# Kernel tuning notes

Measured on AMD Instinct MI355X. Metric: run time of the kernel, lower is better.

## Reference

```python
import jax, jax.numpy as jnp
import numpy as np

N_NODES = 50000
N_EDGES = 800000
D_IN = 128
D_OUT = 128


def setup_inputs() -> dict:
    key = jax.random.key(0)
    ks = jax.random.split(key, 10)
    x = jax.random.normal(ks[0], (N_NODES, D_IN), dtype=jnp.float32)
    lp_rows = jax.random.randint(ks[1], (N_EDGES,), 0, N_NODES, dtype=jnp.int32)
    lp_cols = jax.random.randint(ks[2], (N_EDGES,), 0, N_NODES, dtype=jnp.int32)
    # low-pass operator: positive normalized-adjacency-like weights
    lp_vals = jax.random.uniform(ks[3], (N_EDGES,), dtype=jnp.float32) / 16.0
    hp_rows = jax.random.randint(ks[4], (N_EDGES,), 0, N_NODES, dtype=jnp.int32)
    hp_cols = jax.random.randint(ks[5], (N_EDGES,), 0, N_NODES, dtype=jnp.int32)
    # high-pass operator: signed (Laplacian-like) weights
    hp_vals = jax.random.normal(ks[6], (N_EDGES,), dtype=jnp.float32) / 16.0
    alpha_w = jax.random.normal(ks[7], (1, D_IN), dtype=jnp.float32) * 0.05
    alpha_b = jnp.zeros((1,), dtype=jnp.float32)
    W = jax.random.normal(ks[8], (D_OUT, D_IN), dtype=jnp.float32) * (1.0 / np.sqrt(D_IN))
    b = jnp.zeros((D_OUT,), dtype=jnp.float32)
    return {"x": x, "lp_rows": lp_rows, "lp_cols": lp_cols, "lp_vals": lp_vals,
            "hp_rows": hp_rows, "hp_cols": hp_cols, "hp_vals": hp_vals,
            "alpha_w": alpha_w, "alpha_b": alpha_b, "W": W, "b": b}


def _spmm(rows, cols, vals, x, n):
    # COO sparse-dense matmul: out[r] += vals[e] * x[cols[e]]
    return jax.ops.segment_sum(vals[:, None] * x[cols], rows, num_segments=n)


def reference(x, lp_rows, lp_cols, lp_vals, hp_rows, hp_cols, hp_vals,
              alpha_w, alpha_b, W, b):
    n = x.shape[0]
    # per-node mixing gate: alpha_i = sigmoid(x_i . theta + b)  -> [N, 1]
    alpha = jax.nn.sigmoid(x @ alpha_w.T + alpha_b)
    z_lp = _spmm(lp_rows, lp_cols, lp_vals, x, n)   # [N, D_IN]
    z_hp = _spmm(hp_rows, hp_cols, hp_vals, x, n)   # [N, D_IN]
    z_mix = alpha * z_lp + (1.0 - alpha) * z_hp
    out = jax.nn.relu(z_mix @ W.T + b)              # use_activation=True
    return out, alpha
```

## Files before the change

### kernel.cpp

```cpp
#include <hip/hip_runtime.h>

#define N_NODES_C 50000
#define N_EDGES_C 800000
#define N_EDGES2_C (2 * N_EDGES_C)
#define D 128
#define NSHARD 8
#define SCAP 16
#define OFCAP 4096

#define GNODES 64
#define GP 16
#define LDP 132
#define GRID ((N_NODES_C + GNODES - 1) / GNODES)
#define EPB ((N_EDGES2_C + GRID - 1) / GRID)

static __device__ __forceinline__ unsigned short f2bf(float f) {
  unsigned u = __float_as_uint(f);
  u += 0x7fff + ((u >> 16) & 1);
  return (unsigned short)(u >> 16);
}
static __device__ __forceinline__ float bf_lo(unsigned u) {
  return __uint_as_float(u << 16);
}
static __device__ __forceinline__ float bf_hi(unsigned u) {
  return __uint_as_float(u & 0xffff0000u);
}

static __device__ __forceinline__ int xcd_id() {
  int v;
  asm volatile("s_getreg_b32 %0, hwreg(HW_REG_XCC_ID, 0, 4)" : "=s"(v));
  return v & (NSHARD - 1);
}

__global__ __launch_bounds__(256) void alpha_kernel(
    const float* __restrict__ x,
    const float* __restrict__ aw,
    const float* __restrict__ ab,
    float* __restrict__ alpha_out,
    float* __restrict__ alpha_ws,
    int n) {
  int wave = (int)((blockIdx.x * blockDim.x + threadIdx.x) >> 6);
  int lane = threadIdx.x & 63;
  if (wave >= n) return;
  const float* xr = x + (size_t)wave * D;
  float s = xr[lane] * aw[lane] + xr[lane + 64] * aw[lane + 64];
  #pragma unroll
  for (int off = 32; off > 0; off >>= 1)
    s += __shfl_down(s, off);
  if (lane == 0) {
    float a = 1.0f / (1.0f + __expf(-(s + ab[0])));
    alpha_out[wave] = a;
    alpha_ws[wave] = a;
  }
}

__global__ __launch_bounds__(256) void gemm_fill_kernel(
    const float* __restrict__ x,
    const float* __restrict__ W,
    unsigned* __restrict__ y,
    const int* __restrict__ lp_rows, const int* __restrict__ lp_cols,
    const float* __restrict__ lp_vals,
    const int* __restrict__ hp_rows, const int* __restrict__ hp_cols,
    const float* __restrict__ hp_vals,
    const float* __restrict__ alpha,
    int* __restrict__ rcursor,
    unsigned* __restrict__ pairs,
    int* __restrict__ ofcnt,
    uint2* __restrict__ ofl,
    int n) {
  __shared__ float wt[64][LDP];
  __shared__ float zs[GP][LDP];

  int t = threadIdx.x;
  int node0 = blockIdx.x * GNODES;

  int tj = t >> 3;
  int ns = t & 7;
  int jl = tj * 2;

  for (int jh = 0; jh < 2; ++jh) {
    __syncthreads();
    #pragma unroll
    for (int it = 0; it < 8; ++it) {
      int f = t + it * 256;
      int j = f >> 5;
      int k4 = f & 31;
      *(float4*)&wt[j][k4 * 4] =
          ((const float4*)W)[(size_t)(jh * 64 + j) * 32 + k4];
    }

    for (int p = 0; p < 4; ++p) {
      int nb = node0 + p * GP;
      __syncthreads();
      #pragma unroll
      for (int it = 0; it < 2; ++it) {
        int f = t + it * 256;
        int r = f >> 5;
        int c4 = f & 31;
        int node = nb + r;
        float4 v = make_float4(0.f, 0.f, 0.f, 0.f);
        if (node < n) v = ((const float4*)(x + (size_t)node * D))[c4];
        *(float4*)&zs[r][c4 * 4] = v;
      }
      __syncthreads();

      float acc[2][2] = {};
      #pragma unroll 4
      for (int k = 0; k < D; k += 4) {
        float4 w0 = *(const float4*)&wt[jl][k];
        float4 w1 = *(const float4*)&wt[jl + 1][k];
        float4 z0 = *(const float4*)&zs[ns * 2 + 0][k];
        float4 z1 = *(const float4*)&zs[ns * 2 + 1][k];
        acc[0][0] += z0.x * w0.x + z0.y * w0.y + z0.z * w0.z + z0.w * w0.w;
        acc[0][1] += z0.x * w1.x + z0.y * w1.y + z0.z * w1.z + z0.w * w1.w;
        acc[1][0] += z1.x * w0.x + z1.y * w0.y + z1.z * w0.z + z1.w * w0.w;
        acc[1][1] += z1.x * w1.x + z1.y * w1.y + z1.z * w1.z + z1.w * w1.w;
      }

      #pragma unroll
      for (int ii = 0; ii < 2; ++ii) {
        int node = nb + ns * 2 + ii;
        if (node < n) {
          unsigned o = (unsigned)f2bf(acc[ii][0]) |
                       ((unsigned)f2bf(acc[ii][1]) << 16);
          y[(size_t)node * 64 + jh * 32 + tj] = o;
        }
      }
    }
  }

  int xcc = xcd_id();
  int e0 = blockIdx.x * EPB;
  int e1 = e0 + EPB;
  if (e1 > N_EDGES2_C) e1 = N_EDGES2_C;
  for (int e = e0 + t; e < e1; e += 256) {
    int r, c;
    float v;
    if (e < N_EDGES_C) {
      r = lp_rows[e];
      c = lp_cols[e];
      v = lp_vals[e] * alpha[r];
    } else {
      int i = e - N_EDGES_C;
      r = hp_rows[i];
      c = hp_cols[i];
      v = hp_vals[i] * (1.0f - alpha[r]);
    }
    int p = atomicAdd(&rcursor[xcc * N_NODES_C + r], 1);
    if (p < SCAP) {
      unsigned pk = (unsigned)c | ((unsigned)f2bf(v) << 16);
      pairs[((size_t)r << 7) + (xcc << 4) + p] = pk;
    } else {
      int q = atomicAdd(ofcnt, 1);
      if (q < OFCAP)
        ofl[q] = make_uint2(((unsigned)r << 16) | (unsigned)c,
                            (unsigned)__float_as_int(v));
    }
  }
}

__global__ __launch_bounds__(256) void gather_kernel(
    const int* __restrict__ rcursor,
    const unsigned* __restrict__ pairs,
    const unsigned* __restrict__ y,
    const float* __restrict__ bias,
    const int* __restrict__ ofcnt,
    const uint2* __restrict__ ofl,
    float* __restrict__ out) {
  __shared__ float2 part[4][64];
  int t = threadIdx.x;
  int w = t >> 6;
  int lane = t & 63;
  int row = blockIdx.x * 2 + (w >> 1);
  int half = w & 1;

  float aL = 0.f, aH = 0.f;
  if (row < N_NODES_C) {
    const unsigned* rp = pairs + ((size_t)row << 7) + (half << 6);
    unsigned wsrc = rp[lane];

    #pragma unroll
    for (int sc = 0; sc < 4; ++sc) {
      int s = half * 4 + sc;
      int ds = rcursor[(size_t)s * N_NODES_C + row];
      if (ds > SCAP) ds = SCAP;
      int base = sc << 4;
      int p = 0;
      for (; p + 1 < ds; p += 2) {
        unsigned pk0 = (unsigned)__shfl((int)wsrc, base + p);
        unsigned pk1 = (unsigned)__shfl((int)wsrc, base + p + 1);
        unsigned u0 = y[(size_t)(pk0 & 0xffffu) * 64 + lane];
        unsigned u1 = y[(size_t)(pk1 & 0xffffu) * 64 + lane];
        float v0 = bf_hi(pk0);
        float v1 = bf_hi(pk1);
        aL += v0 * bf_lo(u0) + v1 * bf_lo(u1);
        aH += v0 * bf_hi(u0) + v1 * bf_hi(u1);
      }
      if (p < ds) {
        unsigned pk = (unsigned)__shfl((int)wsrc, base + p);
        unsigned u = y[(size_t)(pk & 0xffffu) * 64 + lane];
        aL += bf_hi(pk) * bf_lo(u);
        aH += bf_hi(pk) * bf_hi(u);
      }
    }

    if (half == 0) {
      int nof = *ofcnt;
      if (nof > OFCAP) nof = OFCAP;
      for (int i = 0; i < nof; ++i) {
        uint2 o = ofl[i];
        if ((int)(o.x >> 16) == row) {
          unsigned u = y[(size_t)(o.x & 0xffffu) * 64 + lane];
          float v = __int_as_float((int)o.y);
          aL += v * bf_lo(u);
          aH += v * bf_hi(u);
        }
      }
    }
  }
  part[w][lane] = make_float2(aL, aH);
  __syncthreads();

  if (half == 0 && row < N_NODES_C) {
    float2 a = part[w][lane];
    float2 b = part[w + 1][lane];
    float2 bv = *(const float2*)&bias[lane * 2];
    float2 o;
    o.x = fmaxf(a.x + b.x + bv.x, 0.0f);
    o.y = fmaxf(a.y + b.y + bv.y, 0.0f);
    *(float2*)&out[(size_t)row * D + lane * 2] = o;
  }
}

extern "C" void kernel_launch(void* const* d_in, const int* in_sizes, int n_in,
                              void* d_out, int out_size, void* d_ws, size_t ws_size,
                              hipStream_t stream) {
  const float* x = (const float*)d_in[0];
  const int* lp_rows = (const int*)d_in[1];
  const int* lp_cols = (const int*)d_in[2];
  const float* lp_vals = (const float*)d_in[3];
  const int* hp_rows = (const int*)d_in[4];
  const int* hp_cols = (const int*)d_in[5];
  const float* hp_vals = (const float*)d_in[6];
  const float* alpha_w = (const float*)d_in[7];
  const float* alpha_b = (const float*)d_in[8];
  const float* W = (const float*)d_in[9];
  const float* bias = (const float*)d_in[10];

  float* out = (float*)d_out;
  float* alpha_out = out + (size_t)N_NODES_C * D;

  char* ws = (char*)d_ws;
  unsigned* y = (unsigned*)ws;   ws += (size_t)N_NODES_C * 64 * 4;
  float* alpha_ws = (float*)ws;  ws += 200192;
  int* rcursor = (int*)ws;       ws += (size_t)N_NODES_C * NSHARD * 4;
  int* ofcnt = (int*)ws;         ws += 256;
  uint2* ofl = (uint2*)ws;       ws += (size_t)OFCAP * 8;
  unsigned* pairs = (unsigned*)ws;
  ws += (size_t)N_NODES_C * NSHARD * SCAP * 4;

  hipMemsetAsync(rcursor, 0,
                 (size_t)N_NODES_C * NSHARD * sizeof(int) + 256, stream);

  alpha_kernel<<<(N_NODES_C + 3) / 4, 256, 0, stream>>>(
      x, alpha_w, alpha_b, alpha_out, alpha_ws, N_NODES_C);

  gemm_fill_kernel<<<GRID, 256, 0, stream>>>(
      x, W, y,
      lp_rows, lp_cols, lp_vals, hp_rows, hp_cols, hp_vals,
      alpha_ws, rcursor, pairs, ofcnt, ofl, N_NODES_C);

  gather_kernel<<<(N_NODES_C + 1) / 2, 256, 0, stream>>>(
      rcursor, pairs, (const unsigned*)y, bias, ofcnt, ofl, out);
}
```

Measured before the change: 319.1 us.

## Split fused GEMM/fill kernel and retile GEMM to 4x4 register blocks

Splits the combined projection-and-edge-bucketing kernel into a dedicated GEMM kernel and a separate fill kernel with its own grid of 2048 blocks. The GEMM now loads all 64 node rows into shared memory once and computes a 4x4 output block per thread, which raises the work per shared-memory load and writes 64-bit packed bf16 results. The aim is better register reuse and occupancy tuned to each phase. The cost is an extra kernel launch, the loss of overlap between GEMM and edge scatter inside one block, and more shared memory per GEMM block.

```diff
diff --git a/kernel.cpp b/kernel.cpp
--- a/kernel.cpp
+++ b/kernel.cpp
@@ -9,10 +9,10 @@
 #define OFCAP 4096
 
 #define GNODES 64
-#define GP 16
 #define LDP 132
-#define GRID ((N_NODES_C + GNODES - 1) / GNODES)
-#define EPB ((N_EDGES2_C + GRID - 1) / GRID)
+#define GGRID ((N_NODES_C + GNODES - 1) / GNODES)
+#define FGRID 2048
+#define FEPB ((N_EDGES2_C + FGRID - 1) / FGRID)
 
 static __device__ __forceinline__ unsigned short f2bf(float f) {
   unsigned u = __float_as_uint(f);
@@ -54,10 +54,86 @@
   }
 }
 
-__global__ __launch_bounds__(256) void gemm_fill_kernel(
+__global__ __launch_bounds__(256) void gemm_kernel(
     const float* __restrict__ x,
     const float* __restrict__ W,
     unsigned* __restrict__ y,
+    int n) {
+  __shared__ float zs[GNODES][LDP];
+  __shared__ float wt[64][LDP];
+
+  int t = threadIdx.x;
+  int node0 = blockIdx.x * GNODES;
+  int tn = t & 15;
+  int tjg = t >> 4;
+  int jb = tjg * 4;
+
+  #pragma unroll
+  for (int it = 0; it < 8; ++it) {
+    int f = t + it * 256;
+    int r = f >> 5;
+    int c4 = f & 31;
+    int node = node0 + r;
+    float4 v = make_float4(0.f, 0.f, 0.f, 0.f);
+    if (node < n) v = ((const float4*)(x + (size_t)node * D))[c4];
+    *(float4*)&zs[r][c4 * 4] = v;
+  }
+
+  for (int jh = 0; jh < 2; ++jh) {
+    if (jh) __syncthreads();
+    #pragma unroll
+    for (int it = 0; it < 8; ++it) {
+      int f = t + it * 256;
+      int j = f >> 5;
+      int k4 = f & 31;
+      *(float4*)&wt[j][k4 * 4] =
+          ((const float4*)W)[(size_t)(jh * 64 + j) * 32 + k4];
+    }
+    __syncthreads();
+
+    float acc[4][4] = {};
+    #pragma unroll 2
+    for (int k = 0; k < D; k += 4) {
+      float4 w0 = *(const float4*)&wt[jb + 0][k];
+      float4 w1 = *(const float4*)&wt[jb + 1][k];
+      float4 w2 = *(const float4*)&wt[jb + 2][k];
+      float4 w3 = *(const float4*)&wt[jb + 3][k];
+      float4 z0 = *(const float4*)&zs[tn][k];
+      float4 z1 = *(const float4*)&zs[tn + 16][k];
+      float4 z2 = *(const float4*)&zs[tn + 32][k];
+      float4 z3 = *(const float4*)&zs[tn + 48][k];
+      acc[0][0] += z0.x*w0.x + z0.y*w0.y + z0.z*w0.z + z0.w*w0.w;
+      acc[0][1] += z0.x*w1.x + z0.y*w1.y + z0.z*w1.z + z0.w*w1.w;
+      acc[0][2] += z0.x*w2.x + z0.y*w2.y + z0.z*w2.z + z0.w*w2.w;
+      acc[0][3] += z0.x*w3.x + z0.y*w3.y + z0.z*w3.z + z0.w*w3.w;
+      acc[1][0] += z1.x*w0.x + z1.y*w0.y + z1.z*w0.z + z1.w*w0.w;
+      acc[1][1] += z1.x*w1.x + z1.y*w1.y + z1.z*w1.z + z1.w*w1.w;
+      acc[1][2] += z1.x*w2.x + z1.y*w2.y + z1.z*w2.z + z1.w*w2.w;
+      acc[1][3] += z1.x*w3.x + z1.y*w3.y + z1.z*w3.z + z1.w*w3.w;
+      acc[2][0] += z2.x*w0.x + z2.y*w0.y + z2.z*w0.z + z2.w*w0.w;
+      acc[2][1] += z2.x*w1.x + z2.y*w1.y + z2.z*w1.z + z2.w*w1.w;
+      acc[2][2] += z2.x*w2.x + z2.y*w2.y + z2.z*w2.z + z2.w*w2.w;
+      acc[2][3] += z2.x*w3.x + z2.y*w3.y + z2.z*w3.z + z2.w*w3.w;
+      acc[3][0] += z3.x*w0.x + z3.y*w0.y + z3.z*w0.z + z3.w*w0.w;
+      acc[3][1] += z3.x*w1.x + z3.y*w1.y + z3.z*w1.z + z3.w*w1.w;
+      acc[3][2] += z3.x*w2.x + z3.y*w2.y + z3.z*w2.z + z3.w*w2.w;
+      acc[3][3] += z3.x*w3.x + z3.y*w3.y + z3.z*w3.z + z3.w*w3.w;
+    }
+
+    #pragma unroll
+    for (int ii = 0; ii < 4; ++ii) {
+      int node = node0 + ii * 16 + tn;
+      if (node < n) {
+        uint2 o;
+        o.x = (unsigned)f2bf(acc[ii][0]) | ((unsigned)f2bf(acc[ii][1]) << 16);
+        o.y = (unsigned)f2bf(acc[ii][2]) | ((unsigned)f2bf(acc[ii][3]) << 16);
+        *(uint2*)&y[(size_t)node * 64 + jh * 32 + tjg * 2] = o;
+      }
+    }
+  }
+}
+
+__global__ __launch_bounds__(256) void fill_kernel(
     const int* __restrict__ lp_rows, const int* __restrict__ lp_cols,
     const float* __restrict__ lp_vals,
     const int* __restrict__ hp_rows, const int* __restrict__ hp_cols,
@@ -66,72 +142,11 @@
     int* __restrict__ rcursor,
     unsigned* __restrict__ pairs,
     int* __restrict__ ofcnt,
-    uint2* __restrict__ ofl,
-    int n) {
-  __shared__ float wt[64][LDP];
-  __shared__ float zs[GP][LDP];
-
+    uint2* __restrict__ ofl) {
+  int xcc = xcd_id();
   int t = threadIdx.x;
-  int node0 = blockIdx.x * GNODES;
-
-  int tj = t >> 3;
-  int ns = t & 7;
-  int jl = tj * 2;
-
-  for (int jh = 0; jh < 2; ++jh) {
-    __syncthreads();
-    #pragma unroll
-    for (int it = 0; it < 8; ++it) {
-      int f = t + it * 256;
-      int j = f >> 5;
-      int k4 = f & 31;
-      *(float4*)&wt[j][k4 * 4] =
-          ((const float4*)W)[(size_t)(jh * 64 + j) * 32 + k4];
-    }
-
-    for (int p = 0; p < 4; ++p) {
-      int nb = node0 + p * GP;
-      __syncthreads();
-      #pragma unroll
-      for (int it = 0; it < 2; ++it) {
-        int f = t + it * 256;
-        int r = f >> 5;
-        int c4 = f & 31;
-        int node = nb + r;
-        float4 v = make_float4(0.f, 0.f, 0.f, 0.f);
-        if (node < n) v = ((const float4*)(x + (size_t)node * D))[c4];
-        *(float4*)&zs[r][c4 * 4] = v;
-      }
-      __syncthreads();
-
-      float acc[2][2] = {};
-      #pragma unroll 4
-      for (int k = 0; k < D; k += 4) {
-        float4 w0 = *(const float4*)&wt[jl][k];
-        float4 w1 = *(const float4*)&wt[jl + 1][k];
-        float4 z0 = *(const float4*)&zs[ns * 2 + 0][k];
-        float4 z1 = *(const float4*)&zs[ns * 2 + 1][k];
-        acc[0][0] += z0.x * w0.x + z0.y * w0.y + z0.z * w0.z + z0.w * w0.w;
-        acc[0][1] += z0.x * w1.x + z0.y * w1.y + z0.z * w1.z + z0.w * w1.w;
-        acc[1][0] += z1.x * w0.x + z1.y * w0.y + z1.z * w0.z + z1.w * w0.w;
-        acc[1][1] += z1.x * w1.x + z1.y * w1.y + z1.z * w1.z + z1.w * w1.w;
-      }
-
-      #pragma unroll
-      for (int ii = 0; ii < 2; ++ii) {
-        int node = nb + ns * 2 + ii;
-        if (node < n) {
-          unsigned o = (unsigned)f2bf(acc[ii][0]) |
-                       ((unsigned)f2bf(acc[ii][1]) << 16);
-          y[(size_t)node * 64 + jh * 32 + tj] = o;
-        }
-      }
-    }
-  }
-
-  int xcc = xcd_id();
-  int e0 = blockIdx.x * EPB;
-  int e1 = e0 + EPB;
+  int e0 = blockIdx.x * FEPB;
+  int e1 = e0 + FEPB;
   if (e1 > N_EDGES2_C) e1 = N_EDGES2_C;
   for (int e = e0 + t; e < e1; e += 256) {
     int r, c;
@@ -265,10 +280,11 @@
   alpha_kernel<<<(N_NODES_C + 3) / 4, 256, 0, stream>>>(
       x, alpha_w, alpha_b, alpha_out, alpha_ws, N_NODES_C);
 
-  gemm_fill_kernel<<<GRID, 256, 0, stream>>>(
-      x, W, y,
+  gemm_kernel<<<GGRID, 256, 0, stream>>>(x, W, y, N_NODES_C);
+
+  fill_kernel<<<FGRID, 256, 0, stream>>>(
       lp_rows, lp_cols, lp_vals, hp_rows, hp_cols, hp_vals,
-      alpha_ws, rcursor, pairs, ofcnt, ofl, N_NODES_C);
+      alpha_ws, rcursor, pairs, ofcnt, ofl);
 
   gather_kernel<<<(N_NODES_C + 1) / 2, 256, 0, stream>>>(
       rcursor, pairs, (const unsigned*)y, bias, ofcnt, ofl, out);
```

After: 314.8 us. No clear change (-1.3%).
